# Optimization experiments

Measured on AMD Instinct MI355X. Metric: run time of the kernel, lower is better.

The kernel has to match this reference:

```python
import jax, jax.numpy as jnp
import numpy as np

TOP_K = 2

def setup_inputs() -> dict:
    key = jax.random.key(0)
    ks = jax.random.split(key, 8)
    B, S, H, E, F = 4, 2048, 1024, 8, 2048  # F = hidden * expansion(2)
    scale_in = 0.02
    return {
        "x": jax.random.normal(ks[0], (B, S, H), dtype=jnp.float32),
        "router_w": jax.random.normal(ks[1], (H, E), dtype=jnp.float32) * scale_in,
        "router_b": jnp.zeros((E,), dtype=jnp.float32),
        "w1": jax.random.normal(ks[2], (E, H, F), dtype=jnp.float32) * scale_in,
        "b1": jnp.zeros((E, F), dtype=jnp.float32),
        "w2": jax.random.normal(ks[3], (E, F, H), dtype=jnp.float32) * scale_in,
        "b2": jnp.zeros((E, H), dtype=jnp.float32),
    }

def reference(x, router_w, router_b, w1, b1, w2, b2):
    B, S, H = x.shape
    E = router_b.shape[0]
    T = B * S
    flat = x.reshape(T, H)
    # Router + top-k gating (softmax over the k selected logits, as in torch code)
    logits = flat @ router_w + router_b                       # [T, E]
    topk_scores, topk_idx = jax.lax.top_k(logits, TOP_K)      # [T, k]
    probs = jax.nn.softmax(topk_scores, axis=-1)              # [T, k]
    # Dense gate matrix: gates[t, e] = prob if e selected for token t else 0
    gates = jnp.zeros((T, E), dtype=flat.dtype).at[
        jnp.arange(T)[:, None], topk_idx
    ].add(probs)                                              # [T, E]
    # Expert FFNs computed as batched GEMMs over the expert axis
    h = jax.nn.relu(jnp.einsum('td,edf->etf', flat, w1) + b1[:, None, :])  # [E, T, F]
    eout = jnp.einsum('etf,efd->etd', h, w2) + b2[:, None, :]              # [E, T, H]
    out = jnp.einsum('etd,te->td', eout, gates)                            # [T, H]
    return out.reshape(B, S, H)
```

## Files before the change

### kernel.cpp

```cpp
#include <hip/hip_runtime.h>
#include <hip/hip_bf16.h>

#define T_TOK 8192
#define HDIM 1024
#define FDIM 2048
#define NEXP 8
#define NASSIGN (T_TOK * 2)
#define ROWCAP (NASSIGN + 256)
#define NHB 64

typedef __bf16 bf16;
typedef __bf16 bf16x4 __attribute__((ext_vector_type(4)));
typedef __bf16 bf16x8 __attribute__((ext_vector_type(8)));
typedef float f32x4 __attribute__((ext_vector_type(4)));

__device__ __forceinline__ void gload_lds16(const void* g, void* l) {
    __builtin_amdgcn_global_load_lds(
        (const __attribute__((address_space(1))) void*)(uintptr_t)g,
        (__attribute__((address_space(3))) void*)(uintptr_t)l,
        16, 0, 0);
}

__global__ __launch_bounds__(256) void transpose_to_bf16(
    const float* __restrict__ in, bf16* __restrict__ out, int R, int C) {
    __shared__ float tile[64][68];
    int e = blockIdx.z;
    const float* inp = in + (size_t)e * R * C;
    bf16* outp = out + (size_t)e * R * C;
    int c0 = blockIdx.x * 64, r0 = blockIdx.y * 64;
    int tid = threadIdx.x;
    int tx = tid & 15, ty = tid >> 4;
#pragma unroll
    for (int i = 0; i < 4; i++) {
        int row = ty + i * 16;
        float4 v = *(const float4*)&inp[(size_t)(r0 + row) * C + c0 + tx * 4];
        *(float4*)&tile[row][tx * 4] = v;
    }
    __syncthreads();
#pragma unroll
    for (int i = 0; i < 2; i++) {
        int idx = tid + i * 256;
        int c = idx >> 3, seg = idx & 7;
        bf16x8 v;
#pragma unroll
        for (int j = 0; j < 8; j++) v[j] = (bf16)tile[seg * 8 + j][c];
        *(bf16x8*)&outp[(size_t)(c0 + c) * R + r0 + seg * 8] = v;
    }
}

__global__ __launch_bounds__(256) void router_kernel(
    const float* __restrict__ x, const float* __restrict__ rw,
    const float* __restrict__ rb, int* __restrict__ expert_pair,
    float2* __restrict__ gate_pair) {
    __shared__ float rwT[NEXP][HDIM];
    __shared__ float rbs[NEXP];
    int tid = threadIdx.x;
    for (int i = tid; i < HDIM * NEXP / 4; i += 256) {
        float4 v = ((const float4*)rw)[i];
        int h = i >> 1, e0 = (i & 1) * 4;
        rwT[e0 + 0][h] = v.x;
        rwT[e0 + 1][h] = v.y;
        rwT[e0 + 2][h] = v.z;
        rwT[e0 + 3][h] = v.w;
    }
    if (tid < NEXP) rbs[tid] = rb[tid];
    __syncthreads();
    int wave = tid >> 6, lane = tid & 63;
    int tbase = blockIdx.x * 32 + wave * 8;

    for (int tk = 0; tk < 8; tk++) {
        int t = tbase + tk;
        const float4* xt = (const float4*)(x + (size_t)t * HDIM);
        float p[NEXP];
#pragma unroll
        for (int e = 0; e < NEXP; e++) p[e] = 0.f;
#pragma unroll
        for (int it = 0; it < 4; it++) {
            float4 v = xt[it * 64 + lane];
            int h = (it * 64 + lane) * 4;
#pragma unroll
            for (int e = 0; e < NEXP; e++) {
                float4 wv = *(const float4*)&rwT[e][h];
                p[e] += v.x * wv.x + v.y * wv.y + v.z * wv.z + v.w * wv.w;
            }
        }
#pragma unroll
        for (int off = 32; off >= 1; off >>= 1) {
#pragma unroll
            for (int e = 0; e < NEXP; e++) p[e] += __shfl_xor(p[e], off, 64);
        }
        if (lane == 0) {
            float lg[NEXP];
#pragma unroll
            for (int e = 0; e < NEXP; e++) lg[e] = p[e] + rbs[e];
            int e0 = 0;
#pragma unroll
            for (int e = 1; e < NEXP; e++)
                if (lg[e] > lg[e0]) e0 = e;
            int e1 = -1;
#pragma unroll
            for (int e = 0; e < NEXP; e++) {
                if (e == e0) continue;
                if (e1 < 0 || lg[e] > lg[e1]) e1 = e;
            }
            float z = expf(lg[e1] - lg[e0]);
            expert_pair[t] = e0 | (e1 << 16);
            gate_pair[t] = make_float2(1.f / (1.f + z), z / (1.f + z));
        }
    }
}

__global__ __launch_bounds__(256) void hist_kernel(
    const int* __restrict__ expert_pair, int* __restrict__ hist) {
    int tid = threadIdx.x;
    int wave = tid >> 6, lane = tid & 63;
    int a = blockIdx.x * 256 + tid;
    int t = a >> 1, j = a & 1;
    int e = (expert_pair[t] >> (16 * j)) & 0xffff;
    __shared__ int wcnt[4][NEXP];
#pragma unroll
    for (int ee = 0; ee < NEXP; ee++) {
        unsigned long long m = __ballot(e == ee);
        if (lane == 0) wcnt[wave][ee] = __popcll(m);
    }
    __syncthreads();
    if (tid < NEXP)
        hist[blockIdx.x * NEXP + tid] =
            wcnt[0][tid] + wcnt[1][tid] + wcnt[2][tid] + wcnt[3][tid];
}

__global__ __launch_bounds__(256) void scan_kernel(
    const int* __restrict__ hist, int* __restrict__ start,
    int* __restrict__ cnt, int* __restrict__ offs) {
    __shared__ int h[NHB * NEXP];
    __shared__ int tot[NEXP];
    __shared__ int offsh[NEXP];
    int tid = threadIdx.x;
    for (int i = tid; i < NHB * NEXP; i += 256) h[i] = hist[i];
    __syncthreads();
    if (tid < NEXP) {
        int s = 0;
        for (int b = 0; b < NHB; b++) s += h[b * NEXP + tid];
        tot[tid] = s;
        cnt[tid] = s;
    }
    __syncthreads();
    if (tid == 0) {
        int o = 0;
        for (int e = 0; e < NEXP; e++) {
            offsh[e] = o;
            offs[e] = o;
            o += tot[e];
        }
    }
    __syncthreads();
    if (tid < NEXP) {
        int run = offsh[tid];
        for (int b = 0; b < NHB; b++) {
            start[b * NEXP + tid] = run;
            run += h[b * NEXP + tid];
        }
    }
}

__global__ __launch_bounds__(256) void scatter_kernel(
    const int* __restrict__ expert_pair, const float2* __restrict__ gate_pair,
    const int* __restrict__ start, int* __restrict__ perm,
    float* __restrict__ gatebuf, int* __restrict__ rowbuf) {
    int tid = threadIdx.x;
    int wave = tid >> 6, lane = tid & 63;
    int a = blockIdx.x * 256 + tid;
    int t = a >> 1, j = a & 1;
    int e = (expert_pair[t] >> (16 * j)) & 0xffff;
    float2 gp = gate_pair[t];
    float g = j ? gp.y : gp.x;
    __shared__ int wcnt[4][NEXP];
    int rankw = 0;
    unsigned long long below = (1ull << lane) - 1ull;
#pragma unroll
    for (int ee = 0; ee < NEXP; ee++) {
        unsigned long long m = __ballot(e == ee);
        if (lane == 0) wcnt[wave][ee] = __popcll(m);
        if (ee == e) rankw = __popcll(m & below);
    }
    __syncthreads();
    int cross = 0;
    for (int w = 0; w < wave; w++) cross += wcnt[w][e];
    int pos = start[blockIdx.x * NEXP + e] + cross + rankw;
    perm[pos] = t;
    gatebuf[pos] = g;
    rowbuf[a] = pos;
}

__global__ __launch_bounds__(256) void pack_kernel(
    const float* __restrict__ x, const int* __restrict__ perm,
    bf16* __restrict__ xg) {
    int r0 = blockIdx.x * 16;
    int wave = threadIdx.x >> 6, lane = threadIdx.x & 63;
#pragma unroll
    for (int i = 0; i < 4; i++) {
        int row = r0 + wave * 4 + i;
        int tok = perm[row];
        const float* src = x + (size_t)tok * HDIM;
        bf16* dst = xg + (size_t)row * HDIM;
#pragma unroll
        for (int it = 0; it < 4; it++) {
            int c = (it * 64 + lane) * 4;
            float4 v = *(const float4*)&src[c];
            bf16x4 b = {(bf16)v.x, (bf16)v.y, (bf16)v.z, (bf16)v.w};
            *(bf16x4*)&dst[c] = b;
        }
    }
}

template <bool RELU, bool GATE>
__global__ __launch_bounds__(256, 2) void moe_gemm(
    const bf16* __restrict__ A, const bf16* __restrict__ B,
    const float* __restrict__ bias, const float* __restrict__ gates,
    bf16* __restrict__ out, const int* __restrict__ cnt,
    const int* __restrict__ offs, int K, int N) {
    int e = blockIdx.z;
    int n_cnt = cnt[e];
    int m0 = blockIdx.y * 128;
    if (m0 >= n_cnt) return;
    int n0 = blockIdx.x * 128;

    __shared__ bf16 As[2 * 128 * 64];
    __shared__ bf16 Bs[2 * 128 * 64];

    int tid = threadIdx.x;
    int lane = tid & 63;
    int wave = tid >> 6;
    int wm = (wave & 1) * 64, wn = (wave >> 1) * 64;
    int quad = lane >> 4;
    int l16 = lane & 15;

    int off_e = offs[e];
    const bf16* Ae = A + (size_t)off_e * K;
    const bf16* Be = B + (size_t)e * N * K;

    int srow = lane >> 3;
    int sseg = (lane & 7) ^ srow;
    const bf16* ag = Ae + (size_t)(m0 + wave * 8 + srow) * K + sseg * 8;
    const bf16* bg = Be + (size_t)(n0 + wave * 8 + srow) * K + sseg * 8;
    bf16* al = As + wave * 8 * 64;
    bf16* bl = Bs + wave * 8 * 64;

    f32x4 acc[4][4];
#pragma unroll
    for (int i = 0; i < 4; i++)
#pragma unroll
        for (int j = 0; j < 4; j++) acc[i][j] = f32x4{0.f, 0.f, 0.f, 0.f};

    int nk = K >> 6;

#pragma unroll
    for (int i = 0; i < 4; i++) {
        gload_lds16(ag + (size_t)(i * 32) * K, al + i * 32 * 64);
        gload_lds16(bg + (size_t)(i * 32) * K, bl + i * 32 * 64);
    }
    __syncthreads();

    int swz = l16 & 7;
    for (int kt = 0; kt < nk; kt++) {
        int cur = kt & 1;
        if (kt + 1 < nk) {
            const bf16* ag2 = ag + (size_t)(kt + 1) * 64;
            const bf16* bg2 = bg + (size_t)(kt + 1) * 64;
            bf16* al2 = al + (cur ^ 1) * (128 * 64);
            bf16* bl2 = bl + (cur ^ 1) * (128 * 64);
#pragma unroll
            for (int i = 0; i < 4; i++) {
                gload_lds16(ag2 + (size_t)(i * 32) * K, al2 + i * 32 * 64);
                gload_lds16(bg2 + (size_t)(i * 32) * K, bl2 + i * 32 * 64);
            }
        }
        const bf16* ac = As + cur * (128 * 64);
        const bf16* bc = Bs + cur * (128 * 64);
#pragma unroll
        for (int kk = 0; kk < 2; kk++) {
            int sg = ((kk * 4 + quad) ^ swz) * 8;
            bf16x8 af[4], bfr[4];
#pragma unroll
            for (int i = 0; i < 4; i++)
                af[i] = *(const bf16x8*)&ac[(wm + i * 16 + l16) * 64 + sg];
#pragma unroll
            for (int j = 0; j < 4; j++)
                bfr[j] = *(const bf16x8*)&bc[(wn + j * 16 + l16) * 64 + sg];
#pragma unroll
            for (int i = 0; i < 4; i++)
#pragma unroll
                for (int j = 0; j < 4; j++)
                    acc[i][j] = __builtin_amdgcn_mfma_f32_16x16x32_bf16(
                        af[i], bfr[j], acc[i][j], 0, 0, 0);
        }
        __syncthreads();
    }

#pragma unroll
    for (int i = 0; i < 4; i++)
#pragma unroll
        for (int j = 0; j < 4; j++)
#pragma unroll
            for (int r = 0; r < 4; r++) {
                int m = m0 + wm + i * 16 + quad * 4 + r;
                if (m < n_cnt) {
                    int n = n0 + wn + j * 16 + l16;
                    float v = acc[i][j][r] + bias[e * N + n];
                    if (RELU) v = v > 0.f ? v : 0.f;
                    if (GATE) v *= gates[off_e + m];
                    out[(size_t)(off_e + m) * N + n] = (bf16)v;
                }
            }
}

__global__ __launch_bounds__(256) void combine_kernel(
    const bf16* __restrict__ eout, const int* __restrict__ rowbuf,
    float* __restrict__ out) {
    int t = blockIdx.x;
    int r0 = rowbuf[2 * t], r1 = rowbuf[2 * t + 1];
    const bf16* p0 = eout + (size_t)r0 * HDIM;
    const bf16* p1 = eout + (size_t)r1 * HDIM;
    float* o = out + (size_t)t * HDIM;
    int n = threadIdx.x * 4;
    bf16x4 a = *(const bf16x4*)&p0[n];
    bf16x4 b = *(const bf16x4*)&p1[n];
    float4 v = {(float)a[0] + (float)b[0], (float)a[1] + (float)b[1],
                (float)a[2] + (float)b[2], (float)a[3] + (float)b[3]};
    *(float4*)&o[n] = v;
}

extern "C" void kernel_launch(void* const* d_in, const int* in_sizes, int n_in,
                              void* d_out, int out_size, void* d_ws, size_t ws_size,
                              hipStream_t stream) {
    const float* x = (const float*)d_in[0];
    const float* rw = (const float*)d_in[1];
    const float* rb = (const float*)d_in[2];
    const float* w1 = (const float*)d_in[3];
    const float* b1 = (const float*)d_in[4];
    const float* w2 = (const float*)d_in[5];
    const float* b2 = (const float*)d_in[6];
    float* out = (float*)d_out;

    char* ws = (char*)d_ws;
    size_t o = 0;
    auto alloc = [&](size_t bytes) {
        char* p = ws + o;
        o += (bytes + 255) & ~(size_t)255;
        return p;
    };
    bf16* w1t = (bf16*)alloc((size_t)NEXP * FDIM * HDIM * 2);
    bf16* w2t = (bf16*)alloc((size_t)NEXP * HDIM * FDIM * 2);
    bf16* hbuf = (bf16*)alloc((size_t)ROWCAP * FDIM * 2);
    bf16* xg = (bf16*)alloc((size_t)ROWCAP * HDIM * 2);
    bf16* eout = xg;
    int* expert_pair = (int*)alloc((size_t)T_TOK * 4);
    float2* gate_pair = (float2*)alloc((size_t)T_TOK * 8);
    int* hist = (int*)alloc((size_t)NHB * NEXP * 4);
    int* start = (int*)alloc((size_t)NHB * NEXP * 4);
    int* perm = (int*)alloc((size_t)NASSIGN * 4);
    float* gatebuf = (float*)alloc((size_t)NASSIGN * 4);
    int* rowbuf = (int*)alloc((size_t)NASSIGN * 4);
    int* cnt = (int*)alloc(256);
    int* offs = (int*)alloc(256);

    transpose_to_bf16<<<dim3(FDIM / 64, HDIM / 64, NEXP), 256, 0, stream>>>(w1, w1t, HDIM, FDIM);
    transpose_to_bf16<<<dim3(HDIM / 64, FDIM / 64, NEXP), 256, 0, stream>>>(w2, w2t, FDIM, HDIM);
    router_kernel<<<T_TOK / 32, 256, 0, stream>>>(x, rw, rb, expert_pair, gate_pair);
    hist_kernel<<<NHB, 256, 0, stream>>>(expert_pair, hist);
    scan_kernel<<<1, 256, 0, stream>>>(hist, start, cnt, offs);
    scatter_kernel<<<NHB, 256, 0, stream>>>(expert_pair, gate_pair, start, perm, gatebuf, rowbuf);
    pack_kernel<<<NASSIGN / 16, 256, 0, stream>>>(x, perm, xg);
    moe_gemm<true, false><<<dim3(FDIM / 128, T_TOK / 128, NEXP), 256, 0, stream>>>(
        xg, w1t, b1, nullptr, hbuf, cnt, offs, HDIM, FDIM);
    moe_gemm<false, true><<<dim3(HDIM / 128, T_TOK / 128, NEXP), 256, 0, stream>>>(
        hbuf, w2t, b2, gatebuf, eout, cnt, offs, FDIM, HDIM);
    combine_kernel<<<T_TOK, 256, 0, stream>>>(eout, rowbuf, out);
}
```

Measured before the change: 488.8 us.

## Compact MoE GEMM grid via tile list, XCD-aware remap, and deeper async prefetch

The scan kernel now emits a compact list of (expert, m-tile) pairs, and both MoE GEMMs launch a 1D grid over active tiles only, so the many empty blocks of the old 3D grid no longer launch. Block IDs are remapped so consecutive work items land on the same XCD, which is meant to improve L2 reuse of weight tiles. The K loop now keeps two global-to-LDS stages in flight, using explicit vmcnt waits and raw barriers in place of __syncthreads. The hand-written waitcnt and barrier sequence carries a risk of ordering mistakes on LDS reuse.

```diff
diff --git a/kernel.cpp b/kernel.cpp
--- a/kernel.cpp
+++ b/kernel.cpp
@@ -8,6 +8,7 @@
 #define NASSIGN (T_TOK * 2)
 #define ROWCAP (NASSIGN + 256)
 #define NHB 64
+#define MAXT 136
 
 typedef __bf16 bf16;
 typedef __bf16 bf16x4 __attribute__((ext_vector_type(4)));
@@ -131,7 +132,9 @@
 
 __global__ __launch_bounds__(256) void scan_kernel(
     const int* __restrict__ hist, int* __restrict__ start,
-    int* __restrict__ cnt, int* __restrict__ offs) {
+    int* __restrict__ cnt, int* __restrict__ offs,
+    int* __restrict__ tile_e, int* __restrict__ tile_m,
+    int* __restrict__ ntiles) {
     __shared__ int h[NHB * NEXP];
     __shared__ int tot[NEXP];
     __shared__ int offsh[NEXP];
@@ -152,6 +155,16 @@
             offs[e] = o;
             o += tot[e];
         }
+        int idx = 0;
+        for (int e = 0; e < NEXP; e++) {
+            int nt = (tot[e] + 127) >> 7;
+            for (int m = 0; m < nt; m++) {
+                tile_e[idx] = e;
+                tile_m[idx] = m;
+                idx++;
+            }
+        }
+        ntiles[0] = idx;
     }
     __syncthreads();
     if (tid < NEXP) {
@@ -213,17 +226,29 @@
     }
 }
 
-template <bool RELU, bool GATE>
+template <bool RELU, bool GATE, int NT>
 __global__ __launch_bounds__(256, 2) void moe_gemm(
     const bf16* __restrict__ A, const bf16* __restrict__ B,
     const float* __restrict__ bias, const float* __restrict__ gates,
     bf16* __restrict__ out, const int* __restrict__ cnt,
-    const int* __restrict__ offs, int K, int N) {
-    int e = blockIdx.z;
+    const int* __restrict__ offs, const int* __restrict__ tile_e,
+    const int* __restrict__ tile_m, const int* __restrict__ ntiles,
+    int K, int N) {
+    int ntl = ntiles[0];
+    int nact = ntl * NT;
+    int f = blockIdx.x;
+    if (f >= nact) return;
+    int q = nact >> 3, r = nact & 7;
+    int xcd = f & 7, rest = f >> 3;
+    int wg = (xcd < r) ? (xcd * (q + 1) + rest)
+                       : (r * (q + 1) + (xcd - r) * q + rest);
+    int tile = wg / NT;
+    int ncol = wg - tile * NT;
+    int e = tile_e[tile];
     int n_cnt = cnt[e];
-    int m0 = blockIdx.y * 128;
-    if (m0 >= n_cnt) return;
-    int n0 = blockIdx.x * 128;
+    int off_e = offs[e];
+    int m0 = tile_m[tile] * 128;
+    int n0 = ncol * 128;
 
     __shared__ bf16 As[2 * 128 * 64];
     __shared__ bf16 Bs[2 * 128 * 64];
@@ -235,7 +260,6 @@
     int quad = lane >> 4;
     int l16 = lane & 15;
 
-    int off_e = offs[e];
     const bf16* Ae = A + (size_t)off_e * K;
     const bf16* Be = B + (size_t)e * N * K;
 
@@ -246,6 +270,18 @@
     bf16* al = As + wave * 8 * 64;
     bf16* bl = Bs + wave * 8 * 64;
 
+    auto stage = [&](int buf, int kt) {
+        const bf16* a = ag + (size_t)kt * 64;
+        const bf16* b = bg + (size_t)kt * 64;
+        bf16* la = al + buf * (128 * 64);
+        bf16* lb = bl + buf * (128 * 64);
+#pragma unroll
+        for (int i = 0; i < 4; i++) {
+            gload_lds16(a + (size_t)(i * 32) * K, la + i * 32 * 64);
+            gload_lds16(b + (size_t)(i * 32) * K, lb + i * 32 * 64);
+        }
+    };
+
     f32x4 acc[4][4];
 #pragma unroll
     for (int i = 0; i < 4; i++)
@@ -253,28 +289,15 @@
         for (int j = 0; j < 4; j++) acc[i][j] = f32x4{0.f, 0.f, 0.f, 0.f};
 
     int nk = K >> 6;
-
-#pragma unroll
-    for (int i = 0; i < 4; i++) {
-        gload_lds16(ag + (size_t)(i * 32) * K, al + i * 32 * 64);
-        gload_lds16(bg + (size_t)(i * 32) * K, bl + i * 32 * 64);
-    }
-    __syncthreads();
-
     int swz = l16 & 7;
+
+    stage(0, 0);
+    stage(1, 1);
+    asm volatile("s_waitcnt vmcnt(8)" ::: "memory");
+    asm volatile("s_barrier" ::: "memory");
+
     for (int kt = 0; kt < nk; kt++) {
         int cur = kt & 1;
-        if (kt + 1 < nk) {
-            const bf16* ag2 = ag + (size_t)(kt + 1) * 64;
-            const bf16* bg2 = bg + (size_t)(kt + 1) * 64;
-            bf16* al2 = al + (cur ^ 1) * (128 * 64);
-            bf16* bl2 = bl + (cur ^ 1) * (128 * 64);
-#pragma unroll
-            for (int i = 0; i < 4; i++) {
-                gload_lds16(ag2 + (size_t)(i * 32) * K, al2 + i * 32 * 64);
-                gload_lds16(bg2 + (size_t)(i * 32) * K, bl2 + i * 32 * 64);
-            }
-        }
         const bf16* ac = As + cur * (128 * 64);
         const bf16* bc = Bs + cur * (128 * 64);
 #pragma unroll
@@ -294,7 +317,14 @@
                     acc[i][j] = __builtin_amdgcn_mfma_f32_16x16x32_bf16(
                         af[i], bfr[j], acc[i][j], 0, 0, 0);
         }
-        __syncthreads();
+        asm volatile("s_barrier" ::: "memory");
+        if (kt + 2 < nk) {
+            stage(cur, kt + 2);
+            asm volatile("s_waitcnt vmcnt(8)" ::: "memory");
+        } else {
+            asm volatile("s_waitcnt vmcnt(0)" ::: "memory");
+        }
+        asm volatile("s_barrier" ::: "memory");
     }
 
 #pragma unroll
@@ -302,11 +332,11 @@
 #pragma unroll
         for (int j = 0; j < 4; j++)
 #pragma unroll
-            for (int r = 0; r < 4; r++) {
-                int m = m0 + wm + i * 16 + quad * 4 + r;
+            for (int r2 = 0; r2 < 4; r2++) {
+                int m = m0 + wm + i * 16 + quad * 4 + r2;
                 if (m < n_cnt) {
                     int n = n0 + wn + j * 16 + l16;
-                    float v = acc[i][j][r] + bias[e * N + n];
+                    float v = acc[i][j][r2] + bias[e * N + n];
                     if (RELU) v = v > 0.f ? v : 0.f;
                     if (GATE) v *= gates[off_e + m];
                     out[(size_t)(off_e + m) * N + n] = (bf16)v;
@@ -363,17 +393,20 @@
     int* rowbuf = (int*)alloc((size_t)NASSIGN * 4);
     int* cnt = (int*)alloc(256);
     int* offs = (int*)alloc(256);
+    int* tile_e = (int*)alloc((size_t)MAXT * 4);
+    int* tile_m = (int*)alloc((size_t)MAXT * 4);
+    int* ntiles = (int*)alloc(256);
 
     transpose_to_bf16<<<dim3(FDIM / 64, HDIM / 64, NEXP), 256, 0, stream>>>(w1, w1t, HDIM, FDIM);
     transpose_to_bf16<<<dim3(HDIM / 64, FDIM / 64, NEXP), 256, 0, stream>>>(w2, w2t, FDIM, HDIM);
     router_kernel<<<T_TOK / 32, 256, 0, stream>>>(x, rw, rb, expert_pair, gate_pair);
     hist_kernel<<<NHB, 256, 0, stream>>>(expert_pair, hist);
-    scan_kernel<<<1, 256, 0, stream>>>(hist, start, cnt, offs);
+    scan_kernel<<<1, 256, 0, stream>>>(hist, start, cnt, offs, tile_e, tile_m, ntiles);
     scatter_kernel<<<NHB, 256, 0, stream>>>(expert_pair, gate_pair, start, perm, gatebuf, rowbuf);
     pack_kernel<<<NASSIGN / 16, 256, 0, stream>>>(x, perm, xg);
-    moe_gemm<true, false><<<dim3(FDIM / 128, T_TOK / 128, NEXP), 256, 0, stream>>>(
-        xg, w1t, b1, nullptr, hbuf, cnt, offs, HDIM, FDIM);
-    moe_gemm<false, true><<<dim3(HDIM / 128, T_TOK / 128, NEXP), 256, 0, stream>>>(
-        hbuf, w2t, b2, gatebuf, eout, cnt, offs, FDIM, HDIM);
+    moe_gemm<true, false, FDIM / 128><<<dim3(MAXT * (FDIM / 128)), 256, 0, stream>>>(
+        xg, w1t, b1, nullptr, hbuf, cnt, offs, tile_e, tile_m, ntiles, HDIM, FDIM);
+    moe_gemm<false, true, HDIM / 128><<<dim3(MAXT * (HDIM / 128)), 256, 0, stream>>>(
+        hbuf, w2t, b2, gatebuf, eout, cnt, offs, tile_e, tile_m, ntiles, FDIM, HDIM);
     combine_kernel<<<T_TOK, 256, 0, stream>>>(eout, rowbuf, out);
 }
```

Result: faster. 469.3 us (-4.0%).
